# Performance work log

Measured on AMD Instinct MI355X. Metric: run time of the kernel, lower is better.

Reference implementation:

```python
import jax, jax.numpy as jnp
import numpy as np

BETA = 0.904837
V_TH = 1.0
SURR_K = 25.0


def _spike(v):
    # Heaviside forward; surrogate gradient irrelevant for fwd-only.
    return (v >= V_TH).astype(v.dtype)


def setup_inputs() -> dict:
    key = jax.random.key(0)
    k1, k2 = jax.random.split(key)
    B, T, H = 16, 1024, 2048
    input_current = jax.random.normal(k1, (B, T, H), dtype=jnp.float32)
    v_init = jax.random.normal(k2, (B, H), dtype=jnp.float32)
    return {"input_current": input_current, "v_init": v_init}


def reference(input_current, v_init):
    # input_current: (B, T, H), v_init: (B, H)
    def step(carry, i_t):
        v, s_prev = carry
        v = BETA * v * (1.0 - s_prev) + i_t  # hard reset via (1 - s_prev)
        s = _spike(v)
        return (v, s), (s, v)

    s0 = jnp.zeros_like(v_init)
    # scan over time axis: move T to leading dim
    (v_final, _), (spikes_t, membrane_t) = jax.lax.scan(
        step, (v_init, s0), jnp.swapaxes(input_current, 0, 1)
    )
    spikes = jnp.swapaxes(spikes_t, 0, 1)      # (B, T, H)
    membrane = jnp.swapaxes(membrane_t, 0, 1)  # (B, T, H)
    return spikes, membrane, v_final
```

## Files before the change

### kernel.cpp

```cpp
#include <hip/hip_runtime.h>


constexpr int B_ = 16;
constexpr int T_ = 1024;
constexpr int H_ = 2048;
constexpr float BETA = 0.904837f;
constexpr int U = 16;

__global__ __launch_bounds__(64) void lif_fwd_kernel(
    const float* __restrict__ in,
    const float* __restrict__ v0,
    float* __restrict__ sp,
    float* __restrict__ mem,
    float* __restrict__ vf)
{
    const int idx = blockIdx.x * 64 + threadIdx.x;
    const int b = idx >> 11;
    const int h = idx & (H_ - 1);
    const size_t base = (size_t)b * T_ * H_ + (size_t)h;
    const float* __restrict__ ip = in + base;

    float v = v0[idx];
    float s = 0.0f;

    float cur[U];
#pragma unroll
    for (int j = 0; j < U; ++j) cur[j] = ip[(size_t)j * H_];

    int t0 = 0;
    for (; t0 < T_ - U; t0 += U) {
        float nxt[U];
#pragma unroll
        for (int j = 0; j < U; ++j) nxt[j] = ip[(size_t)(t0 + U + j) * H_];

#pragma unroll
        for (int j = 0; j < U; ++j) {
            v = BETA * v * (1.0f - s) + cur[j];
            s = (v >= 1.0f) ? 1.0f : 0.0f;
            const size_t o = base + (size_t)(t0 + j) * H_;
            sp[o] = s;
            mem[o] = v;
        }

#pragma unroll
        for (int j = 0; j < U; ++j) cur[j] = nxt[j];
    }

#pragma unroll
    for (int j = 0; j < U; ++j) {
        v = BETA * v * (1.0f - s) + cur[j];
        s = (v >= 1.0f) ? 1.0f : 0.0f;
        const size_t o = base + (size_t)(t0 + j) * H_;
        sp[o] = s;
        mem[o] = v;
    }

    vf[idx] = v;
}

extern "C" void kernel_launch(void* const* d_in, const int* in_sizes, int n_in,
                              void* d_out, int out_size, void* d_ws, size_t ws_size,
                              hipStream_t stream) {
    const float* in = (const float*)d_in[0];
    const float* v0 = (const float*)d_in[1];

    float* out = (float*)d_out;
    const size_t n_bth = (size_t)B_ * T_ * H_;
    float* sp  = out;
    float* mem = out + n_bth;
    float* vf  = out + 2 * n_bth;

    const int threads = B_ * H_;
    const int block = 64;
    const int grid = threads / block;
    lif_fwd_kernel<<<grid, block, 0, stream>>>(in, v0, sp, mem, vf);
}
```

Before: 367.5 us.

## Vectorize LIF scan to float2 per thread with nontemporal loads/stores

Each thread now handles two adjacent neurons using float2 loads and stores, halving the thread count and doubling access width. Global traffic uses nontemporal load/store builtins to avoid polluting caches with streaming data. The prefetch buffer becomes a rolling ring, refilled slot by slot inside the compute loop instead of through a separate next array. With half as many wavefronts (256 blocks of 64 threads), latency hiding may suffer on a GPU with many CUs.

Result: slower. 385.7 us (+4.9%).

```diff
diff --git a/kernel.cpp b/kernel.cpp
--- a/kernel.cpp
+++ b/kernel.cpp
@@ -4,73 +4,89 @@
 constexpr int B_ = 16;
 constexpr int T_ = 1024;
 constexpr int H_ = 2048;
+constexpr int H2 = H_ / 2;
 constexpr float BETA = 0.904837f;
-constexpr int U = 16;
+constexpr int D = 16;
+
+typedef __attribute__((ext_vector_type(2))) float fx2;
 
 __global__ __launch_bounds__(64) void lif_fwd_kernel(
-    const float* __restrict__ in,
-    const float* __restrict__ v0,
-    float* __restrict__ sp,
-    float* __restrict__ mem,
-    float* __restrict__ vf)
+    const fx2* __restrict__ in,
+    const fx2* __restrict__ v0,
+    fx2* __restrict__ sp,
+    fx2* __restrict__ mem,
+    fx2* __restrict__ vf)
 {
     const int idx = blockIdx.x * 64 + threadIdx.x;
-    const int b = idx >> 11;
-    const int h = idx & (H_ - 1);
-    const size_t base = (size_t)b * T_ * H_ + (size_t)h;
-    const float* __restrict__ ip = in + base;
+    const int b  = idx >> 10;
+    const int h2 = idx & (H2 - 1);
+    const size_t base = (size_t)b * T_ * H2 + (size_t)h2;
 
-    float v = v0[idx];
-    float s = 0.0f;
+    const fx2* __restrict__ ip = in + base;
+    fx2* __restrict__ spp = sp + base;
+    fx2* __restrict__ mp  = mem + base;
 
-    float cur[U];
+    fx2 vv = v0[idx];
+    float v0r = vv[0], v1r = vv[1];
+    float s0r = 0.0f, s1r = 0.0f;
+
+    fx2 buf[D];
 #pragma unroll
-    for (int j = 0; j < U; ++j) cur[j] = ip[(size_t)j * H_];
+    for (int j = 0; j < D; ++j)
+        buf[j] = __builtin_nontemporal_load(ip + (size_t)j * H2);
 
     int t0 = 0;
-    for (; t0 < T_ - U; t0 += U) {
-        float nxt[U];
+    for (; t0 < T_ - D; t0 += D) {
 #pragma unroll
-        for (int j = 0; j < U; ++j) nxt[j] = ip[(size_t)(t0 + U + j) * H_];
+        for (int j = 0; j < D; ++j) {
+            const fx2 x = buf[j];
+            buf[j] = __builtin_nontemporal_load(ip + (size_t)(t0 + D + j) * H2);
 
-#pragma unroll
-        for (int j = 0; j < U; ++j) {
-            v = BETA * v * (1.0f - s) + cur[j];
-            s = (v >= 1.0f) ? 1.0f : 0.0f;
-            const size_t o = base + (size_t)(t0 + j) * H_;
-            sp[o] = s;
-            mem[o] = v;
+            v0r = BETA * v0r * (1.0f - s0r) + x[0];
+            v1r = BETA * v1r * (1.0f - s1r) + x[1];
+            s0r = (v0r >= 1.0f) ? 1.0f : 0.0f;
+            s1r = (v1r >= 1.0f) ? 1.0f : 0.0f;
+
+            const size_t o = (size_t)(t0 + j) * H2;
+            fx2 sv; sv[0] = s0r; sv[1] = s1r;
+            fx2 mv; mv[0] = v0r; mv[1] = v1r;
+            __builtin_nontemporal_store(sv, spp + o);
+            __builtin_nontemporal_store(mv, mp + o);
         }
-
-#pragma unroll
-        for (int j = 0; j < U; ++j) cur[j] = nxt[j];
     }
 
 #pragma unroll
-    for (int j = 0; j < U; ++j) {
-        v = BETA * v * (1.0f - s) + cur[j];
-        s = (v >= 1.0f) ? 1.0f : 0.0f;
-        const size_t o = base + (size_t)(t0 + j) * H_;
-        sp[o] = s;
-        mem[o] = v;
+    for (int j = 0; j < D; ++j) {
+        const fx2 x = buf[j];
+        v0r = BETA * v0r * (1.0f - s0r) + x[0];
+        v1r = BETA * v1r * (1.0f - s1r) + x[1];
+        s0r = (v0r >= 1.0f) ? 1.0f : 0.0f;
+        s1r = (v1r >= 1.0f) ? 1.0f : 0.0f;
+
+        const size_t o = (size_t)(t0 + j) * H2;
+        fx2 sv; sv[0] = s0r; sv[1] = s1r;
+        fx2 mv; mv[0] = v0r; mv[1] = v1r;
+        __builtin_nontemporal_store(sv, spp + o);
+        __builtin_nontemporal_store(mv, mp + o);
     }
 
-    vf[idx] = v;
+    fx2 vfv; vfv[0] = v0r; vfv[1] = v1r;
+    vf[idx] = vfv;
 }
 
 extern "C" void kernel_launch(void* const* d_in, const int* in_sizes, int n_in,
                               void* d_out, int out_size, void* d_ws, size_t ws_size,
                               hipStream_t stream) {
-    const float* in = (const float*)d_in[0];
-    const float* v0 = (const float*)d_in[1];
+    const fx2* in = (const fx2*)d_in[0];
+    const fx2* v0 = (const fx2*)d_in[1];
 
     float* out = (float*)d_out;
     const size_t n_bth = (size_t)B_ * T_ * H_;
-    float* sp  = out;
-    float* mem = out + n_bth;
-    float* vf  = out + 2 * n_bth;
+    fx2* sp  = (fx2*)out;
+    fx2* mem = (fx2*)(out + n_bth);
+    fx2* vf  = (fx2*)(out + 2 * n_bth);
 
-    const int threads = B_ * H_;
+    const int threads = B_ * H2;
     const int block = 64;
     const int grid = threads / block;
     lif_fwd_kernel<<<grid, block, 0, stream>>>(in, v0, sp, mem, vf);
```
